# Kernel optimization log

Measured on AMD Instinct MI355X. Metric: run time of the kernel, lower is better.

The kernel has to match this reference:

```python
import jax, jax.numpy as jnp
import numpy as np

B, E, O, H = 4096, 1024, 16, 1024  # batch, embed_dim, num_ops, hidden_dim


def setup_inputs() -> dict:
    key = jax.random.key(0)
    k1, k2, k3, k4, k5, k6 = jax.random.split(key, 6)
    s1 = 1.0 / np.sqrt(E)
    s2 = 1.0 / np.sqrt(H)
    return {
        "x_aug": jax.random.normal(k1, (B, E), dtype=jnp.float32),
        "op_idx": jax.random.randint(k2, (B,), 0, O, dtype=jnp.int32),
        "W1": jax.random.normal(k3, (E, O, H), dtype=jnp.float32) * s1,  # DenseGeneral kernel: embed -> (ops, hidden)
        "b1": jnp.zeros((O, H), dtype=jnp.float32),
        "W2": jax.random.normal(k4, (H, O, H), dtype=jnp.float32) * s2,  # per-op second layer (diagonal of DenseGeneral)
        "b2": jnp.zeros((O, H), dtype=jnp.float32),
    }


def reference(x_aug, op_idx, W1, b1, W2, b2):
    # h1[b,o,h] = relu(sum_e x[b,e] W1[e,o,h] + b1[o,h])
    h1 = jax.nn.relu(jnp.einsum("be,eoh->boh", x_aug, W1) + b1)
    # h2[b,o,g] = relu(sum_h h1[b,o,h] W2[h,o,g] + b2[o,g])  (per-op MLP)
    h2 = jax.nn.relu(jnp.einsum("boh,hog->bog", h1, W2) + b2)
    # select the chosen operator's output per example
    idx = jnp.broadcast_to(op_idx[:, None, None], (x_aug.shape[0], 1, h2.shape[-1]))
    return jnp.take_along_axis(h2, idx, axis=1).squeeze(1)  # [B, H]
```

## Files before the change

### kernel.cpp

```cpp
#include <hip/hip_runtime.h>

#define Bn 4096
#define En 1024
#define On 16
#define Hn 1024
#define OHn (On * Hn)

#define BM 64
#define BN 128
#define BK 64
#define MAXT 80

using floatx4 = __attribute__((ext_vector_type(4))) float;
using float4v = __attribute__((ext_vector_type(4))) float;
using bf16x8  = __attribute__((ext_vector_type(8))) __bf16;
using short8v = __attribute__((ext_vector_type(8))) short;
using short4v = __attribute__((ext_vector_type(4))) short;

__device__ inline unsigned short f2bf(float f) {
    unsigned u = __builtin_bit_cast(unsigned, f);
    u += 0x7fffu + ((u >> 16) & 1u);
    return (unsigned short)(u >> 16);
}

__device__ __forceinline__ void gld16(const unsigned short* g, unsigned short* l) {
    __builtin_amdgcn_global_load_lds(
        (const __attribute__((address_space(1))) unsigned int*)g,
        (__attribute__((address_space(3))) unsigned int*)l, 16, 0, 0);
}

__global__ void bucket_kernel(const int* __restrict__ op_idx,
                              int* __restrict__ sorted_idx,
                              int* __restrict__ offsets,
                              int* __restrict__ tile_o,
                              int* __restrict__ tile_m) {
    __shared__ int cnt[On], cur[On], off[On + 1];
    int tid = threadIdx.x;
    if (tid < On) { cnt[tid] = 0; cur[tid] = 0; }
    __syncthreads();
    for (int i = tid; i < Bn; i += blockDim.x) atomicAdd(&cnt[op_idx[i]], 1);
    __syncthreads();
    if (tid == 0) {
        int s = 0;
        for (int o = 0; o < On; ++o) { off[o] = s; s += cnt[o]; }
        off[On] = s;
        int nt = 0;
        for (int o = 0; o < On; ++o)
            for (int m0 = 0; m0 < cnt[o]; m0 += BM) { tile_o[nt] = o; tile_m[nt] = m0; ++nt; }
        for (; nt < MAXT; ++nt) { tile_o[nt] = -1; tile_m[nt] = 0; }
    }
    __syncthreads();
    for (int i = tid; i < Bn; i += blockDim.x) {
        int o = op_idx[i];
        int p = off[o] + atomicAdd(&cur[o], 1);
        sorted_idx[p] = i;
    }
    if (tid <= On) offsets[tid] = off[tid];
}

__device__ __forceinline__ void pack_w_block(const float* __restrict__ W,
                                             unsigned short* __restrict__ Wp,
                                             int o, int g, int hblk, int t) {
    int h = hblk * 256 + t;
    const float* src = W + (size_t)(g * 8) * OHn + (size_t)o * Hn + h;
    short8v v;
#pragma unroll
    for (int j = 0; j < 8; ++j) v[j] = (short)f2bf(src[(size_t)j * OHn]);
    *(short8v*)&Wp[(((size_t)o * 128 + g) * Hn + h) * 8] = v;
}

__device__ __forceinline__ void pack_x_block(const float* __restrict__ x,
                                             const int* __restrict__ sorted_idx,
                                             unsigned short* __restrict__ x_s,
                                             int p, int t) {
    int row = sorted_idx[p];
    float4v v = *(const float4v*)(x + (size_t)row * En + t * 4);
    short4v w;
#pragma unroll
    for (int j = 0; j < 4; ++j) w[j] = (short)f2bf(v[j]);
    *(short4v*)&x_s[(size_t)p * En + t * 4] = w;
}

__global__ __launch_bounds__(256) void pack_all_kernel(
    const float* __restrict__ W1, const float* __restrict__ W2,
    const float* __restrict__ x, const int* __restrict__ sorted_idx,
    unsigned short* __restrict__ Wp1, unsigned short* __restrict__ Wp2,
    unsigned short* __restrict__ x_s) {
    int b = blockIdx.x, t = threadIdx.x;
    if (b < 8192) {
        pack_w_block(W1, Wp1, b >> 9, (b >> 2) & 127, b & 3, t);
    } else if (b < 16384) {
        int c = b - 8192;
        pack_w_block(W2, Wp2, c >> 9, (c >> 2) & 127, c & 3, t);
    } else {
        pack_x_block(x, sorted_idx, x_s, b - 16384, t);
    }
}

__global__ __launch_bounds__(256) void pack_x_kernel(const float* __restrict__ x,
                                                     const int* __restrict__ sorted_idx,
                                                     unsigned short* __restrict__ x_s) {
    pack_x_block(x, sorted_idx, x_s, blockIdx.x, threadIdx.x);
}
__global__ __launch_bounds__(256) void pack_w_kernel(const float* __restrict__ W,
                                                     unsigned short* __restrict__ Wp) {
    pack_w_block(W, Wp, blockIdx.z, blockIdx.y, blockIdx.x, threadIdx.x);
}

__global__ __launch_bounds__(256) void gemm1_kernel(
    const unsigned short* __restrict__ x_s, const unsigned short* __restrict__ Wp,
    const float* __restrict__ bias1, const int* __restrict__ offsets,
    const int* __restrict__ tile_o, const int* __restrict__ tile_m,
    unsigned short* __restrict__ h1) {
    int o = tile_o[blockIdx.y];
    if (o < 0) return;
    int m0 = tile_m[blockIdx.y];
    int off = offsets[o];
    int cnt = offsets[o + 1] - off;
    int n0 = blockIdx.x * BN;

    __shared__ __attribute__((aligned(16))) unsigned short As[2][8][BM][8];
    __shared__ __attribute__((aligned(16))) unsigned short Bs[2][8][BN][8];

    int tid = threadIdx.x;

    int arow = tid & 63, ag = tid >> 6;
    int rr = m0 + arow; if (rr >= cnt) rr = cnt - 1;
    const unsigned short* aBase = x_s + (size_t)(off + rr) * En;

    int bn = tid & 127, bg = tid >> 7;
    const unsigned short* bBase = Wp + (((size_t)o * 128 + bg) * Hn + n0 + bn) * 8;

    auto STAGE = [&](int buf, int kt) {
        gld16(aBase + kt + ag * 8,        &As[buf][ag][arow][0]);
        gld16(aBase + kt + (ag + 4) * 8,  &As[buf][ag + 4][arow][0]);
        const unsigned short* bk = bBase + (size_t)kt * Hn;
#pragma unroll
        for (int i = 0; i < 4; ++i)
            gld16(bk + (size_t)i * (2 * Hn * 8), &Bs[buf][bg + 2 * i][bn][0]);
    };

    floatx4 acc[2][4] = {};
    int lane = tid & 63, wave = tid >> 6;
    int wm = (wave >> 1) * 32, wn = (wave & 1) * 64;
    int l15 = lane & 15, kg = lane >> 4;

    auto COMPUTE = [&](int buf) {
#pragma unroll
        for (int ks = 0; ks < 2; ++ks) {
            int g = ks * 4 + kg;
            bf16x8 af[2], bfr[4];
#pragma unroll
            for (int mt = 0; mt < 2; ++mt) af[mt] = *(const bf16x8*)&As[buf][g][wm + mt * 16 + l15][0];
#pragma unroll
            for (int nt = 0; nt < 4; ++nt) bfr[nt] = *(const bf16x8*)&Bs[buf][g][wn + nt * 16 + l15][0];
#pragma unroll
            for (int mt = 0; mt < 2; ++mt)
#pragma unroll
                for (int nt = 0; nt < 4; ++nt)
                    acc[mt][nt] = __builtin_amdgcn_mfma_f32_16x16x32_bf16(af[mt], bfr[nt], acc[mt][nt], 0, 0, 0);
        }
    };

    STAGE(0, 0);
    for (int kt = 0; kt < En; kt += 2 * BK) {
        __syncthreads();
        STAGE(1, kt + BK);
        COMPUTE(0);
        __syncthreads();
        if (kt + 2 * BK < En) STAGE(0, kt + 2 * BK);
        COMPUTE(1);
    }

    int r4 = (lane >> 4) * 4;
#pragma unroll
    for (int nt = 0; nt < 4; ++nt) {
        int col = n0 + wn + nt * 16 + l15;
        float bv = bias1[o * Hn + col];
#pragma unroll
        for (int mt = 0; mt < 2; ++mt) {
#pragma unroll
            for (int r = 0; r < 4; ++r) {
                int row = m0 + wm + mt * 16 + r4 + r;
                if (row < cnt) {
                    float v = acc[mt][nt][r] + bv;
                    v = v > 0.f ? v : 0.f;
                    h1[(size_t)(off + row) * Hn + col] = f2bf(v);
                }
            }
        }
    }
}

__global__ __launch_bounds__(256) void gemm2_kernel(
    const unsigned short* __restrict__ h1, const unsigned short* __restrict__ Wp,
    const float* __restrict__ bias2, const int* __restrict__ sorted_idx,
    const int* __restrict__ offsets, const int* __restrict__ tile_o,
    const int* __restrict__ tile_m, float* __restrict__ out) {
    int o = tile_o[blockIdx.y];
    if (o < 0) return;
    int m0 = tile_m[blockIdx.y];
    int off = offsets[o];
    int cnt = offsets[o + 1] - off;
    int n0 = blockIdx.x * BN;

    __shared__ __attribute__((aligned(16))) unsigned short As[2][8][BM][8];
    __shared__ __attribute__((aligned(16))) unsigned short Bs[2][8][BN][8];

    int tid = threadIdx.x;

    int arow = tid & 63, ag = tid >> 6;
    int rr = m0 + arow; if (rr >= cnt) rr = cnt - 1;
    const unsigned short* aBase = h1 + (size_t)(off + rr) * Hn;

    int bn = tid & 127, bg = tid >> 7;
    const unsigned short* bBase = Wp + (((size_t)o * 128 + bg) * Hn + n0 + bn) * 8;

    auto STAGE = [&](int buf, int kt) {
        gld16(aBase + kt + ag * 8,        &As[buf][ag][arow][0]);
        gld16(aBase + kt + (ag + 4) * 8,  &As[buf][ag + 4][arow][0]);
        const unsigned short* bk = bBase + (size_t)kt * Hn;
#pragma unroll
        for (int i = 0; i < 4; ++i)
            gld16(bk + (size_t)i * (2 * Hn * 8), &Bs[buf][bg + 2 * i][bn][0]);
    };

    floatx4 acc[2][4] = {};
    int lane = tid & 63, wave = tid >> 6;
    int wm = (wave >> 1) * 32, wn = (wave & 1) * 64;
    int l15 = lane & 15, kg = lane >> 4;

    auto COMPUTE = [&](int buf) {
#pragma unroll
        for (int ks = 0; ks < 2; ++ks) {
            int g = ks * 4 + kg;
            bf16x8 af[2], bfr[4];
#pragma unroll
            for (int mt = 0; mt < 2; ++mt) af[mt] = *(const bf16x8*)&As[buf][g][wm + mt * 16 + l15][0];
#pragma unroll
            for (int nt = 0; nt < 4; ++nt) bfr[nt] = *(const bf16x8*)&Bs[buf][g][wn + nt * 16 + l15][0];
#pragma unroll
            for (int mt = 0; mt < 2; ++mt)
#pragma unroll
                for (int nt = 0; nt < 4; ++nt)
                    acc[mt][nt] = __builtin_amdgcn_mfma_f32_16x16x32_bf16(af[mt], bfr[nt], acc[mt][nt], 0, 0, 0);
        }
    };

    STAGE(0, 0);
    for (int kt = 0; kt < Hn; kt += 2 * BK) {
        __syncthreads();
        STAGE(1, kt + BK);
        COMPUTE(0);
        __syncthreads();
        if (kt + 2 * BK < Hn) STAGE(0, kt + 2 * BK);
        COMPUTE(1);
    }

    int r4 = (lane >> 4) * 4;
    float bv[4];
#pragma unroll
    for (int nt = 0; nt < 4; ++nt) bv[nt] = bias2[o * Hn + n0 + wn + nt * 16 + l15];
#pragma unroll
    for (int mt = 0; mt < 2; ++mt) {
#pragma unroll
        for (int r = 0; r < 4; ++r) {
            int row = m0 + wm + mt * 16 + r4 + r;
            if (row < cnt) {
                int b = sorted_idx[off + row];
                float* orow = out + (size_t)b * Hn + n0 + wn + l15;
#pragma unroll
                for (int nt = 0; nt < 4; ++nt) {
                    float v = acc[mt][nt][r] + bv[nt];
                    orow[nt * 16] = v > 0.f ? v : 0.f;
                }
            }
        }
    }
}

extern "C" void kernel_launch(void* const* d_in, const int* in_sizes, int n_in,
                              void* d_out, int out_size, void* d_ws, size_t ws_size,
                              hipStream_t stream) {
    const float* x      = (const float*)d_in[0];
    const int*   op_idx = (const int*)d_in[1];
    const float* W1     = (const float*)d_in[2];
    const float* bias1  = (const float*)d_in[3];
    const float* W2     = (const float*)d_in[4];
    const float* bias2  = (const float*)d_in[5];
    float* out = (float*)d_out;

    char* ws = (char*)d_ws;
    int* offsets    = (int*)ws;
    int* sorted_idx = (int*)(ws + 256);
    int* tile_o     = (int*)(ws + 16640);
    int* tile_m     = (int*)(ws + 17152);

    const size_t HDR       = 32768;
    const size_t X_S_ELEMS = (size_t)Bn * En;
    const size_t H1_ELEMS  = (size_t)Bn * Hn;
    const size_t WP_ELEMS  = (size_t)On * 128 * Hn * 8;
    const size_t need_full = HDR + 2 * (X_S_ELEMS + H1_ELEMS + WP_ELEMS);
    const size_t need_half = HDR + 2 * (X_S_ELEMS + H1_ELEMS + WP_ELEMS) - 2 * WP_ELEMS;

    unsigned short* x_s = (unsigned short*)(ws + HDR);
    unsigned short* h1  = x_s + X_S_ELEMS;
    unsigned short* Wp1 = h1 + H1_ELEMS;
    unsigned short* Wp2 = Wp1 + WP_ELEMS;

    hipLaunchKernelGGL(bucket_kernel, dim3(1), dim3(1024), 0, stream,
                       op_idx, sorted_idx, offsets, tile_o, tile_m);

    dim3 grid_g(Hn / BN, MAXT);
    if (ws_size >= need_full) {
        hipLaunchKernelGGL(pack_all_kernel, dim3(20480), dim3(256), 0, stream,
                           W1, W2, x, sorted_idx, Wp1, Wp2, x_s);
        hipLaunchKernelGGL(gemm1_kernel, grid_g, dim3(256), 0, stream,
                           x_s, Wp1, bias1, offsets, tile_o, tile_m, h1);
        hipLaunchKernelGGL(gemm2_kernel, grid_g, dim3(256), 0, stream,
                           h1, Wp2, bias2, sorted_idx, offsets, tile_o, tile_m, out);
    } else if (ws_size >= need_half) {
        hipLaunchKernelGGL(pack_x_kernel, dim3(Bn), dim3(256), 0, stream,
                           x, sorted_idx, x_s);
        hipLaunchKernelGGL(pack_w_kernel, dim3(Hn / 256, En / 8, On), dim3(256), 0, stream,
                           W1, Wp1);
        hipLaunchKernelGGL(gemm1_kernel, grid_g, dim3(256), 0, stream,
                           x_s, Wp1, bias1, offsets, tile_o, tile_m, h1);
        hipLaunchKernelGGL(pack_w_kernel, dim3(Hn / 256, Hn / 8, On), dim3(256), 0, stream,
                           W2, Wp1);
        hipLaunchKernelGGL(gemm2_kernel, grid_g, dim3(256), 0, stream,
                           h1, Wp1, bias2, sorted_idx, offsets, tile_o, tile_m, out);
    }
}
```

Before: 241.5 us.

## Overlap W2 packing with GEMM1 and vectorize weight packing loads

The W2 fp32-to-bf16 packing moves out of the standalone pack kernel and into extra blocks appended to the gemm1 grid, so that memory-bound work can run alongside the GEMM1 tiles. Weight packing now has each thread load four consecutive h values with float4 loads across 8 k rows, cutting the block count and widening memory accesses. Each x-pack block now handles four rows. The workspace size checks are also corrected to account for both packed weight buffers. The cost is that the padding blocks share gemm1's register and LDS footprint, which may limit how much overlap actually happens.

```diff
diff --git a/kernel.cpp b/kernel.cpp
--- a/kernel.cpp
+++ b/kernel.cpp
@@ -58,71 +58,76 @@
     if (tid <= On) offsets[tid] = off[tid];
 }
 
-__device__ __forceinline__ void pack_w_block(const float* __restrict__ W,
-                                             unsigned short* __restrict__ Wp,
-                                             int o, int g, int hblk, int t) {
-    int h = hblk * 256 + t;
-    const float* src = W + (size_t)(g * 8) * OHn + (size_t)o * Hn + h;
-    short8v v;
-#pragma unroll
-    for (int j = 0; j < 8; ++j) v[j] = (short)f2bf(src[(size_t)j * OHn]);
-    *(short8v*)&Wp[(((size_t)o * 128 + g) * Hn + h) * 8] = v;
-}
-
-__device__ __forceinline__ void pack_x_block(const float* __restrict__ x,
-                                             const int* __restrict__ sorted_idx,
-                                             unsigned short* __restrict__ x_s,
-                                             int p, int t) {
-    int row = sorted_idx[p];
-    float4v v = *(const float4v*)(x + (size_t)row * En + t * 4);
-    short4v w;
-#pragma unroll
-    for (int j = 0; j < 4; ++j) w[j] = (short)f2bf(v[j]);
-    *(short4v*)&x_s[(size_t)p * En + t * 4] = w;
-}
-
-__global__ __launch_bounds__(256) void pack_all_kernel(
-    const float* __restrict__ W1, const float* __restrict__ W2,
-    const float* __restrict__ x, const int* __restrict__ sorted_idx,
-    unsigned short* __restrict__ Wp1, unsigned short* __restrict__ Wp2,
-    unsigned short* __restrict__ x_s) {
+__device__ __forceinline__ void pack_w_block4(const float* __restrict__ W,
+                                              unsigned short* __restrict__ Wp,
+                                              int o, int g, int t) {
+    int h0 = t * 4;
+    const float* src = W + (size_t)(g * 8) * OHn + (size_t)o * Hn + h0;
+    float4v v[8];
+#pragma unroll
+    for (int j = 0; j < 8; ++j) v[j] = *(const float4v*)(src + (size_t)j * OHn);
+    unsigned short* dst = Wp + (((size_t)o * 128 + g) * Hn + h0) * 8;
+#pragma unroll
+    for (int hh = 0; hh < 4; ++hh) {
+        short8v w;
+#pragma unroll
+        for (int j = 0; j < 8; ++j) w[j] = (short)f2bf(v[j][hh]);
+        *(short8v*)(dst + hh * 8) = w;
+    }
+}
+
+__global__ __launch_bounds__(256) void pack1_kernel(
+    const float* __restrict__ W1, const float* __restrict__ x,
+    const int* __restrict__ sorted_idx,
+    unsigned short* __restrict__ Wp1, unsigned short* __restrict__ x_s) {
     int b = blockIdx.x, t = threadIdx.x;
-    if (b < 8192) {
-        pack_w_block(W1, Wp1, b >> 9, (b >> 2) & 127, b & 3, t);
-    } else if (b < 16384) {
-        int c = b - 8192;
-        pack_w_block(W2, Wp2, c >> 9, (c >> 2) & 127, c & 3, t);
+    if (b < 2048) {
+        pack_w_block4(W1, Wp1, b >> 7, b & 127, t);
     } else {
-        pack_x_block(x, sorted_idx, x_s, b - 16384, t);
-    }
-}
-
-__global__ __launch_bounds__(256) void pack_x_kernel(const float* __restrict__ x,
-                                                     const int* __restrict__ sorted_idx,
-                                                     unsigned short* __restrict__ x_s) {
-    pack_x_block(x, sorted_idx, x_s, blockIdx.x, threadIdx.x);
-}
+        int p0 = (b - 2048) * 4;
+#pragma unroll
+        for (int r = 0; r < 4; ++r) {
+            int p = p0 + r;
+            int row = sorted_idx[p];
+            float4v v = *(const float4v*)(x + (size_t)row * En + t * 4);
+            short4v w;
+#pragma unroll
+            for (int j = 0; j < 4; ++j) w[j] = (short)f2bf(v[j]);
+            *(short4v*)&x_s[(size_t)p * En + t * 4] = w;
+        }
+    }
+}
+
 __global__ __launch_bounds__(256) void pack_w_kernel(const float* __restrict__ W,
                                                      unsigned short* __restrict__ Wp) {
-    pack_w_block(W, Wp, blockIdx.z, blockIdx.y, blockIdx.x, threadIdx.x);
+    int b = blockIdx.x;
+    pack_w_block4(W, Wp, b >> 7, b & 127, threadIdx.x);
 }
 
 __global__ __launch_bounds__(256) void gemm1_kernel(
     const unsigned short* __restrict__ x_s, const unsigned short* __restrict__ Wp,
     const float* __restrict__ bias1, const int* __restrict__ offsets,
     const int* __restrict__ tile_o, const int* __restrict__ tile_m,
-    unsigned short* __restrict__ h1) {
-    int o = tile_o[blockIdx.y];
+    unsigned short* __restrict__ h1,
+    const float* __restrict__ W2, unsigned short* __restrict__ Wp2) {
+    int yy = blockIdx.y;
+    int tid = threadIdx.x;
+    if (yy >= MAXT) {
+        if (W2 != nullptr && Wp2 != nullptr) {
+            int p = (yy - MAXT) * 8 + blockIdx.x;
+            pack_w_block4(W2, Wp2, p >> 7, p & 127, tid);
+        }
+        return;
+    }
+    int o = tile_o[yy];
     if (o < 0) return;
-    int m0 = tile_m[blockIdx.y];
+    int m0 = tile_m[yy];
     int off = offsets[o];
     int cnt = offsets[o + 1] - off;
     int n0 = blockIdx.x * BN;
 
     __shared__ __attribute__((aligned(16))) unsigned short As[2][8][BM][8];
     __shared__ __attribute__((aligned(16))) unsigned short Bs[2][8][BN][8];
-
-    int tid = threadIdx.x;
 
     int arow = tid & 63, ag = tid >> 6;
     int rr = m0 + arow; if (rr >= cnt) rr = cnt - 1;
@@ -300,8 +305,8 @@
     const size_t X_S_ELEMS = (size_t)Bn * En;
     const size_t H1_ELEMS  = (size_t)Bn * Hn;
     const size_t WP_ELEMS  = (size_t)On * 128 * Hn * 8;
-    const size_t need_full = HDR + 2 * (X_S_ELEMS + H1_ELEMS + WP_ELEMS);
-    const size_t need_half = HDR + 2 * (X_S_ELEMS + H1_ELEMS + WP_ELEMS) - 2 * WP_ELEMS;
+    const size_t need_full = HDR + 2 * (X_S_ELEMS + H1_ELEMS + 2 * WP_ELEMS);
+    const size_t need_half = HDR + 2 * (X_S_ELEMS + H1_ELEMS + WP_ELEMS);
 
     unsigned short* x_s = (unsigned short*)(ws + HDR);
     unsigned short* h1  = x_s + X_S_ELEMS;
@@ -311,24 +316,22 @@
     hipLaunchKernelGGL(bucket_kernel, dim3(1), dim3(1024), 0, stream,
                        op_idx, sorted_idx, offsets, tile_o, tile_m);
 
-    dim3 grid_g(Hn / BN, MAXT);
     if (ws_size >= need_full) {
-        hipLaunchKernelGGL(pack_all_kernel, dim3(20480), dim3(256), 0, stream,
-                           W1, W2, x, sorted_idx, Wp1, Wp2, x_s);
-        hipLaunchKernelGGL(gemm1_kernel, grid_g, dim3(256), 0, stream,
-                           x_s, Wp1, bias1, offsets, tile_o, tile_m, h1);
-        hipLaunchKernelGGL(gemm2_kernel, grid_g, dim3(256), 0, stream,
+        hipLaunchKernelGGL(pack1_kernel, dim3(3072), dim3(256), 0, stream,
+                           W1, x, sorted_idx, Wp1, x_s);
+        hipLaunchKernelGGL(gemm1_kernel, dim3(Hn / BN, MAXT + 256), dim3(256), 0, stream,
+                           x_s, Wp1, bias1, offsets, tile_o, tile_m, h1, W2, Wp2);
+        hipLaunchKernelGGL(gemm2_kernel, dim3(Hn / BN, MAXT), dim3(256), 0, stream,
                            h1, Wp2, bias2, sorted_idx, offsets, tile_o, tile_m, out);
     } else if (ws_size >= need_half) {
-        hipLaunchKernelGGL(pack_x_kernel, dim3(Bn), dim3(256), 0, stream,
-                           x, sorted_idx, x_s);
-        hipLaunchKernelGGL(pack_w_kernel, dim3(Hn / 256, En / 8, On), dim3(256), 0, stream,
-                           W1, Wp1);
-        hipLaunchKernelGGL(gemm1_kernel, grid_g, dim3(256), 0, stream,
-                           x_s, Wp1, bias1, offsets, tile_o, tile_m, h1);
-        hipLaunchKernelGGL(pack_w_kernel, dim3(Hn / 256, Hn / 8, On), dim3(256), 0, stream,
+        hipLaunchKernelGGL(pack1_kernel, dim3(3072), dim3(256), 0, stream,
+                           W1, x, sorted_idx, Wp1, x_s);
+        hipLaunchKernelGGL(gemm1_kernel, dim3(Hn / BN, MAXT), dim3(256), 0, stream,
+                           x_s, Wp1, bias1, offsets, tile_o, tile_m, h1,
+                           (const float*)nullptr, (unsigned short*)nullptr);
+        hipLaunchKernelGGL(pack_w_kernel, dim3(2048), dim3(256), 0, stream,
                            W2, Wp1);
-        hipLaunchKernelGGL(gemm2_kernel, grid_g, dim3(256), 0, stream,
+        hipLaunchKernelGGL(gemm2_kernel, dim3(Hn / BN, MAXT), dim3(256), 0, stream,
                            h1, Wp1, bias2, sorted_idx, offsets, tile_o, tile_m, out);
     }
 }
```

New measurement: 247.5 us. +2.5%, slower.

## Fuse fp32-to-bf16 weight conversion into GEMM loads, drop weight packing pass

Applied to the files above, without the earlier changes.

Removes the separate kernel that converted W1 and W2 to a packed bf16 layout and instead loads fp32 weights directly in the GEMM kernels, converting in registers before writing to LDS. The goal is to remove the large extra write and re-read of packed weights. In exchange the weights are read in fp32 by each M-tile, which doubles per-tile weight bytes. Staging also switches from async LDS double buffering to register prefetch with a single LDS buffer.

```diff
diff --git a/kernel.cpp b/kernel.cpp
--- a/kernel.cpp
+++ b/kernel.cpp
@@ -21,12 +21,6 @@
     unsigned u = __builtin_bit_cast(unsigned, f);
     u += 0x7fffu + ((u >> 16) & 1u);
     return (unsigned short)(u >> 16);
-}
-
-__device__ __forceinline__ void gld16(const unsigned short* g, unsigned short* l) {
-    __builtin_amdgcn_global_load_lds(
-        (const __attribute__((address_space(1))) unsigned int*)g,
-        (__attribute__((address_space(3))) unsigned int*)l, 16, 0, 0);
 }
 
 __global__ void bucket_kernel(const int* __restrict__ op_idx,
@@ -58,57 +52,25 @@
     if (tid <= On) offsets[tid] = off[tid];
 }
 
-__device__ __forceinline__ void pack_w_block(const float* __restrict__ W,
-                                             unsigned short* __restrict__ Wp,
-                                             int o, int g, int hblk, int t) {
-    int h = hblk * 256 + t;
-    const float* src = W + (size_t)(g * 8) * OHn + (size_t)o * Hn + h;
-    short8v v;
-#pragma unroll
-    for (int j = 0; j < 8; ++j) v[j] = (short)f2bf(src[(size_t)j * OHn]);
-    *(short8v*)&Wp[(((size_t)o * 128 + g) * Hn + h) * 8] = v;
-}
-
-__device__ __forceinline__ void pack_x_block(const float* __restrict__ x,
-                                             const int* __restrict__ sorted_idx,
-                                             unsigned short* __restrict__ x_s,
-                                             int p, int t) {
-    int row = sorted_idx[p];
-    float4v v = *(const float4v*)(x + (size_t)row * En + t * 4);
-    short4v w;
-#pragma unroll
-    for (int j = 0; j < 4; ++j) w[j] = (short)f2bf(v[j]);
-    *(short4v*)&x_s[(size_t)p * En + t * 4] = w;
-}
-
-__global__ __launch_bounds__(256) void pack_all_kernel(
-    const float* __restrict__ W1, const float* __restrict__ W2,
-    const float* __restrict__ x, const int* __restrict__ sorted_idx,
-    unsigned short* __restrict__ Wp1, unsigned short* __restrict__ Wp2,
-    unsigned short* __restrict__ x_s) {
-    int b = blockIdx.x, t = threadIdx.x;
-    if (b < 8192) {
-        pack_w_block(W1, Wp1, b >> 9, (b >> 2) & 127, b & 3, t);
-    } else if (b < 16384) {
-        int c = b - 8192;
-        pack_w_block(W2, Wp2, c >> 9, (c >> 2) & 127, c & 3, t);
-    } else {
-        pack_x_block(x, sorted_idx, x_s, b - 16384, t);
-    }
-}
-
 __global__ __launch_bounds__(256) void pack_x_kernel(const float* __restrict__ x,
                                                      const int* __restrict__ sorted_idx,
                                                      unsigned short* __restrict__ x_s) {
-    pack_x_block(x, sorted_idx, x_s, blockIdx.x, threadIdx.x);
-}
-__global__ __launch_bounds__(256) void pack_w_kernel(const float* __restrict__ W,
-                                                     unsigned short* __restrict__ Wp) {
-    pack_w_block(W, Wp, blockIdx.z, blockIdx.y, blockIdx.x, threadIdx.x);
-}
+    int p0 = blockIdx.x * 4, t = threadIdx.x;
+#pragma unroll
+    for (int r = 0; r < 4; ++r) {
+        int p = p0 + r;
+        int row = sorted_idx[p];
+        float4v v = *(const float4v*)(x + (size_t)row * En + t * 4);
+        short4v w;
+#pragma unroll
+        for (int j = 0; j < 4; ++j) w[j] = (short)f2bf(v[j]);
+        *(short4v*)&x_s[(size_t)p * En + t * 4] = w;
+    }
+}
+
 
 __global__ __launch_bounds__(256) void gemm1_kernel(
-    const unsigned short* __restrict__ x_s, const unsigned short* __restrict__ Wp,
+    const unsigned short* __restrict__ x_s, const float* __restrict__ W,
     const float* __restrict__ bias1, const int* __restrict__ offsets,
     const int* __restrict__ tile_o, const int* __restrict__ tile_m,
     unsigned short* __restrict__ h1) {
@@ -119,8 +81,8 @@
     int cnt = offsets[o + 1] - off;
     int n0 = blockIdx.x * BN;
 
-    __shared__ __attribute__((aligned(16))) unsigned short As[2][8][BM][8];
-    __shared__ __attribute__((aligned(16))) unsigned short Bs[2][8][BN][8];
+    __shared__ __attribute__((aligned(16))) unsigned short As[8][BM][8];
+    __shared__ __attribute__((aligned(16))) unsigned short Bs[8][BN][8];
 
     int tid = threadIdx.x;
 
@@ -128,16 +90,33 @@
     int rr = m0 + arow; if (rr >= cnt) rr = cnt - 1;
     const unsigned short* aBase = x_s + (size_t)(off + rr) * En;
 
-    int bn = tid & 127, bg = tid >> 7;
-    const unsigned short* bBase = Wp + (((size_t)o * 128 + bg) * Hn + n0 + bn) * 8;
-
-    auto STAGE = [&](int buf, int kt) {
-        gld16(aBase + kt + ag * 8,        &As[buf][ag][arow][0]);
-        gld16(aBase + kt + (ag + 4) * 8,  &As[buf][ag + 4][arow][0]);
-        const unsigned short* bk = bBase + (size_t)kt * Hn;
-#pragma unroll
-        for (int i = 0; i < 4; ++i)
-            gld16(bk + (size_t)i * (2 * Hn * 8), &Bs[buf][bg + 2 * i][bn][0]);
+    int o8 = tid >> 5, c4 = (tid & 31) * 4;
+    const float* bBase = W + ((size_t)(o8 * 8) * On + o) * Hn + n0 + c4;
+
+    short8v a_pre[2];
+    float4v b_pre[8];
+
+    auto LOADA = [&](int kt) {
+        a_pre[0] = *(const short8v*)(aBase + kt + ag * 8);
+        a_pre[1] = *(const short8v*)(aBase + kt + (ag + 4) * 8);
+    };
+    auto LOADB = [&](int kt) {
+        const float* p = bBase + (size_t)kt * OHn;
+#pragma unroll
+        for (int j = 0; j < 8; ++j) b_pre[j] = *(const float4v*)(p + (size_t)j * OHn);
+    };
+    int rot = (tid >> 1) & 3;
+    auto WRITE = [&]() {
+        *(short8v*)&As[ag][arow][0]     = a_pre[0];
+        *(short8v*)&As[ag + 4][arow][0] = a_pre[1];
+#pragma unroll
+        for (int cc = 0; cc < 4; ++cc) {
+            int c = (cc + rot) & 3;
+            short8v w;
+#pragma unroll
+            for (int j = 0; j < 8; ++j) w[j] = (short)f2bf(b_pre[j][c]);
+            *(short8v*)&Bs[o8][c4 + c][0] = w;
+        }
     };
 
     floatx4 acc[2][4] = {};
@@ -145,15 +124,15 @@
     int wm = (wave >> 1) * 32, wn = (wave & 1) * 64;
     int l15 = lane & 15, kg = lane >> 4;
 
-    auto COMPUTE = [&](int buf) {
+    auto COMPUTE = [&]() {
 #pragma unroll
         for (int ks = 0; ks < 2; ++ks) {
             int g = ks * 4 + kg;
             bf16x8 af[2], bfr[4];
 #pragma unroll
-            for (int mt = 0; mt < 2; ++mt) af[mt] = *(const bf16x8*)&As[buf][g][wm + mt * 16 + l15][0];
-#pragma unroll
-            for (int nt = 0; nt < 4; ++nt) bfr[nt] = *(const bf16x8*)&Bs[buf][g][wn + nt * 16 + l15][0];
+            for (int mt = 0; mt < 2; ++mt) af[mt] = *(const bf16x8*)&As[g][wm + mt * 16 + l15][0];
+#pragma unroll
+            for (int nt = 0; nt < 4; ++nt) bfr[nt] = *(const bf16x8*)&Bs[g][wn + nt * 16 + l15][0];
 #pragma unroll
             for (int mt = 0; mt < 2; ++mt)
 #pragma unroll
@@ -162,14 +141,14 @@
         }
     };
 
-    STAGE(0, 0);
-    for (int kt = 0; kt < En; kt += 2 * BK) {
+    LOADA(0); LOADB(0);
+    for (int kt = 0; kt < En; kt += BK) {
+        WRITE();
         __syncthreads();
-        STAGE(1, kt + BK);
-        COMPUTE(0);
+        int ktn = kt + BK;
+        if (ktn < En) { LOADA(ktn); LOADB(ktn); }
+        COMPUTE();
         __syncthreads();
-        if (kt + 2 * BK < En) STAGE(0, kt + 2 * BK);
-        COMPUTE(1);
     }
 
     int r4 = (lane >> 4) * 4;
@@ -193,7 +172,7 @@
 }
 
 __global__ __launch_bounds__(256) void gemm2_kernel(
-    const unsigned short* __restrict__ h1, const unsigned short* __restrict__ Wp,
+    const unsigned short* __restrict__ h1, const float* __restrict__ W,
     const float* __restrict__ bias2, const int* __restrict__ sorted_idx,
     const int* __restrict__ offsets, const int* __restrict__ tile_o,
     const int* __restrict__ tile_m, float* __restrict__ out) {
@@ -204,8 +183,8 @@
     int cnt = offsets[o + 1] - off;
     int n0 = blockIdx.x * BN;
 
-    __shared__ __attribute__((aligned(16))) unsigned short As[2][8][BM][8];
-    __shared__ __attribute__((aligned(16))) unsigned short Bs[2][8][BN][8];
+    __shared__ __attribute__((aligned(16))) unsigned short As[8][BM][8];
+    __shared__ __attribute__((aligned(16))) unsigned short Bs[8][BN][8];
 
     int tid = threadIdx.x;
 
@@ -213,16 +192,33 @@
     int rr = m0 + arow; if (rr >= cnt) rr = cnt - 1;
     const unsigned short* aBase = h1 + (size_t)(off + rr) * Hn;
 
-    int bn = tid & 127, bg = tid >> 7;
-    const unsigned short* bBase = Wp + (((size_t)o * 128 + bg) * Hn + n0 + bn) * 8;
-
-    auto STAGE = [&](int buf, int kt) {
-        gld16(aBase + kt + ag * 8,        &As[buf][ag][arow][0]);
-        gld16(aBase + kt + (ag + 4) * 8,  &As[buf][ag + 4][arow][0]);
-        const unsigned short* bk = bBase + (size_t)kt * Hn;
-#pragma unroll
-        for (int i = 0; i < 4; ++i)
-            gld16(bk + (size_t)i * (2 * Hn * 8), &Bs[buf][bg + 2 * i][bn][0]);
+    int o8 = tid >> 5, c4 = (tid & 31) * 4;
+    const float* bBase = W + ((size_t)(o8 * 8) * On + o) * Hn + n0 + c4;
+
+    short8v a_pre[2];
+    float4v b_pre[8];
+
+    auto LOADA = [&](int kt) {
+        a_pre[0] = *(const short8v*)(aBase + kt + ag * 8);
+        a_pre[1] = *(const short8v*)(aBase + kt + (ag + 4) * 8);
+    };
+    auto LOADB = [&](int kt) {
+        const float* p = bBase + (size_t)kt * OHn;
+#pragma unroll
+        for (int j = 0; j < 8; ++j) b_pre[j] = *(const float4v*)(p + (size_t)j * OHn);
+    };
+    int rot = (tid >> 1) & 3;
+    auto WRITE = [&]() {
+        *(short8v*)&As[ag][arow][0]     = a_pre[0];
+        *(short8v*)&As[ag + 4][arow][0] = a_pre[1];
+#pragma unroll
+        for (int cc = 0; cc < 4; ++cc) {
+            int c = (cc + rot) & 3;
+            short8v w;
+#pragma unroll
+            for (int j = 0; j < 8; ++j) w[j] = (short)f2bf(b_pre[j][c]);
+            *(short8v*)&Bs[o8][c4 + c][0] = w;
+        }
     };
 
     floatx4 acc[2][4] = {};
@@ -230,15 +226,15 @@
     int wm = (wave >> 1) * 32, wn = (wave & 1) * 64;
     int l15 = lane & 15, kg = lane >> 4;
 
-    auto COMPUTE = [&](int buf) {
+    auto COMPUTE = [&]() {
 #pragma unroll
         for (int ks = 0; ks < 2; ++ks) {
             int g = ks * 4 + kg;
             bf16x8 af[2], bfr[4];
 #pragma unroll
-            for (int mt = 0; mt < 2; ++mt) af[mt] = *(const bf16x8*)&As[buf][g][wm + mt * 16 + l15][0];
-#pragma unroll
-            for (int nt = 0; nt < 4; ++nt) bfr[nt] = *(const bf16x8*)&Bs[buf][g][wn + nt * 16 + l15][0];
+            for (int mt = 0; mt < 2; ++mt) af[mt] = *(const bf16x8*)&As[g][wm + mt * 16 + l15][0];
+#pragma unroll
+            for (int nt = 0; nt < 4; ++nt) bfr[nt] = *(const bf16x8*)&Bs[g][wn + nt * 16 + l15][0];
 #pragma unroll
             for (int mt = 0; mt < 2; ++mt)
 #pragma unroll
@@ -247,14 +243,14 @@
         }
     };
 
-    STAGE(0, 0);
-    for (int kt = 0; kt < Hn; kt += 2 * BK) {
+    LOADA(0); LOADB(0);
+    for (int kt = 0; kt < Hn; kt += BK) {
+        WRITE();
         __syncthreads();
-        STAGE(1, kt + BK);
-        COMPUTE(0);
+        int ktn = kt + BK;
+        if (ktn < Hn) { LOADA(ktn); LOADB(ktn); }
+        COMPUTE();
         __syncthreads();
-        if (kt + 2 * BK < Hn) STAGE(0, kt + 2 * BK);
-        COMPUTE(1);
     }
 
     int r4 = (lane >> 4) * 4;
@@ -296,39 +292,16 @@
     int* tile_o     = (int*)(ws + 16640);
     int* tile_m     = (int*)(ws + 17152);
 
-    const size_t HDR       = 32768;
-    const size_t X_S_ELEMS = (size_t)Bn * En;
-    const size_t H1_ELEMS  = (size_t)Bn * Hn;
-    const size_t WP_ELEMS  = (size_t)On * 128 * Hn * 8;
-    const size_t need_full = HDR + 2 * (X_S_ELEMS + H1_ELEMS + WP_ELEMS);
-    const size_t need_half = HDR + 2 * (X_S_ELEMS + H1_ELEMS + WP_ELEMS) - 2 * WP_ELEMS;
-
+    const size_t HDR = 32768;
     unsigned short* x_s = (unsigned short*)(ws + HDR);
-    unsigned short* h1  = x_s + X_S_ELEMS;
-    unsigned short* Wp1 = h1 + H1_ELEMS;
-    unsigned short* Wp2 = Wp1 + WP_ELEMS;
+    unsigned short* h1  = x_s + (size_t)Bn * En;
 
     hipLaunchKernelGGL(bucket_kernel, dim3(1), dim3(1024), 0, stream,
                        op_idx, sorted_idx, offsets, tile_o, tile_m);
-
-    dim3 grid_g(Hn / BN, MAXT);
-    if (ws_size >= need_full) {
-        hipLaunchKernelGGL(pack_all_kernel, dim3(20480), dim3(256), 0, stream,
-                           W1, W2, x, sorted_idx, Wp1, Wp2, x_s);
-        hipLaunchKernelGGL(gemm1_kernel, grid_g, dim3(256), 0, stream,
-                           x_s, Wp1, bias1, offsets, tile_o, tile_m, h1);
-        hipLaunchKernelGGL(gemm2_kernel, grid_g, dim3(256), 0, stream,
-                           h1, Wp2, bias2, sorted_idx, offsets, tile_o, tile_m, out);
-    } else if (ws_size >= need_half) {
-        hipLaunchKernelGGL(pack_x_kernel, dim3(Bn), dim3(256), 0, stream,
-                           x, sorted_idx, x_s);
-        hipLaunchKernelGGL(pack_w_kernel, dim3(Hn / 256, En / 8, On), dim3(256), 0, stream,
-                           W1, Wp1);
-        hipLaunchKernelGGL(gemm1_kernel, grid_g, dim3(256), 0, stream,
-                           x_s, Wp1, bias1, offsets, tile_o, tile_m, h1);
-        hipLaunchKernelGGL(pack_w_kernel, dim3(Hn / 256, Hn / 8, On), dim3(256), 0, stream,
-                           W2, Wp1);
-        hipLaunchKernelGGL(gemm2_kernel, grid_g, dim3(256), 0, stream,
-                           h1, Wp1, bias2, sorted_idx, offsets, tile_o, tile_m, out);
-    }
-}
+    hipLaunchKernelGGL(pack_x_kernel, dim3(Bn / 4), dim3(256), 0, stream,
+                       x, sorted_idx, x_s);
+    hipLaunchKernelGGL(gemm1_kernel, dim3(Hn / BN, MAXT), dim3(256), 0, stream,
+                       x_s, W1, bias1, offsets, tile_o, tile_m, h1);
+    hipLaunchKernelGGL(gemm2_kernel, dim3(Hn / BN, MAXT), dim3(256), 0, stream,
+                       h1, W2, bias2, sorted_idx, offsets, tile_o, tile_m, out);
+}
```

Result: slower. 565.0 us (+133.9%).
